# Optimization experiments

Measured on AMD Instinct MI355X. Metric: run time of the kernel, lower is better.

The kernel has to match this reference:

```python
import jax, jax.numpy as jnp
import numpy as np

EPS = 1e-5
HEAD_DIM = 2048 // 32  # embed_dim // num_heads -> scale factor only


def _layernorm(x, w):
    # torch: (x - mean) / sqrt(var_biased + eps) * w  (no bias)
    mean = jnp.mean(x, axis=-1, keepdims=True)
    var = jnp.var(x, axis=-1, keepdims=True)  # unbiased=False
    return w * ((x - mean) / jnp.sqrt(var + EPS))


def setup_inputs() -> dict:
    key = jax.random.key(0)
    ks = jax.random.split(key, 9)
    E, F, B, S = 2048, 8192, 2, 4096
    sE = 1.0 / np.sqrt(E)
    sF = 1.0 / np.sqrt(F)
    return {
        "x": jax.random.normal(ks[0], (B, S, E), jnp.float32),
        "ln_w": jnp.ones((E,), jnp.float32),
        "w_q": jax.random.normal(ks[1], (E, E), jnp.float32) * sE,
        "w_k": jax.random.normal(ks[2], (E, E), jnp.float32) * sE,
        "w_v": jax.random.normal(ks[3], (E, E), jnp.float32) * sE,
        "w_o": jax.random.normal(ks[4], (E, E), jnp.float32) * sE,
        "w_gate": jax.random.normal(ks[5], (E, F), jnp.float32) * sE,
        "w_up": jax.random.normal(ks[6], (E, F), jnp.float32) * sE,
        "w_down": jax.random.normal(ks[7], (F, E), jnp.float32) * sF,
    }


def reference(x, ln_w, w_q, w_k, w_v, w_o, w_gate, w_up, w_down):
    # --- pre-attention LN (uses input_layernorm weight) ---
    residual = x
    h = _layernorm(x, ln_w)  # [b, s, e]

    # --- attention exactly as written: transpose(1,2) WITHOUT head split ---
    q = jnp.einsum("bse,ef->bsf", h, w_q).swapaxes(1, 2)  # [b, e, s]
    k = jnp.einsum("bse,ef->bsf", h, w_k).swapaxes(1, 2)  # [b, e, s]
    v = jnp.einsum("bse,ef->bsf", h, w_v).swapaxes(1, 2)  # [b, e, s]
    # scores over the FEATURE axis: [b, e, e]
    scores = jnp.einsum("bes,bfs->bef", q, k) / np.sqrt(HEAD_DIM)
    weights = jax.nn.softmax(scores, axis=-1)
    attn = jnp.einsum("bef,bfs->bes", weights, v)  # [b, e, s]
    attn = attn.swapaxes(1, 2)  # [b, s, e]
    x = jnp.einsum("bse,ef->bsf", attn, w_o) + residual

    # --- pre-MLP LN: the module reuses input_layernorm here (faithful) ---
    residual = x
    h = _layernorm(x, ln_w)

    # --- GELU-gated FFN (exact erf gelu, torch default) ---
    gate = jax.nn.gelu(jnp.einsum("bse,ef->bsf", h, w_gate), approximate=False)
    up = jnp.einsum("bse,ef->bsf", h, w_up)
    out = jnp.einsum("bsf,fe->bse", gate * up, w_down) + residual
    return out
```

## Files before the change

### kernel.cpp

```cpp
#include <hip/hip_runtime.h>
#include <hip/hip_bf16.h>

typedef __hip_bfloat16 bf16;
typedef __attribute__((ext_vector_type(8))) short bf16x8;
typedef __attribute__((ext_vector_type(4))) float f32x4;

#define EPI_F32 0
#define EPI_BF16 1
#define EPI_BF16_T 2
#define EPI_F32_RES 3
#define EPI_BF16_GELU 4
#define EPI_BF16_MUL 5

__device__ __forceinline__ void gload_lds16(const void* g, void* l) {
  __builtin_amdgcn_global_load_lds(
      (const __attribute__((address_space(1))) unsigned int*)g,
      (__attribute__((address_space(3))) unsigned int*)l, 16, 0, 0);
}

template<int EPI>
__global__ __launch_bounds__(256, 3) void gemm_k(
    const bf16* __restrict__ A, const bf16* __restrict__ B,
    void* __restrict__ Cv, const void* __restrict__ auxv,
    int M, int N, int K, int lda, int ldb,
    long sAz, long sBz, long sCz, int batchM)
{
  __shared__ bf16 As[128 * 64];
  __shared__ bf16 Bs[128 * 64];

  const int z = blockIdx.z;
  A += (size_t)z * (size_t)sAz;
  B += (size_t)z * (size_t)sBz;

  const int brow = blockIdx.y * 128;
  const int bcol = blockIdx.x * 128;
  const int t = threadIdx.x;
  const int w = t >> 6;
  const int lane = t & 63;
  const int wr = (w >> 1) * 64;
  const int wc = (w & 1) * 64;
  const int l15 = lane & 15;
  const int lg = lane >> 4;

  f32x4 acc[4][4];
#pragma unroll
  for (int i = 0; i < 4; ++i)
#pragma unroll
    for (int j = 0; j < 4; ++j) {
      f32x4 zz = {0.f, 0.f, 0.f, 0.f};
      acc[i][j] = zz;
    }

  for (int kt = 0; kt < K; kt += 64) {
#pragma unroll
    for (int i = 0; i < 4; ++i) {
      const int bslot = (i * 4 + w) * 64;
      const int slot = bslot + lane;
      const int r = slot >> 3;
      const int cs = (slot & 7) ^ (r & 7);
      gload_lds16(A + (size_t)(brow + r) * lda + kt + cs * 8, (char*)As + bslot * 16);
      gload_lds16(B + (size_t)(bcol + r) * ldb + kt + cs * 8, (char*)Bs + bslot * 16);
    }
    __syncthreads();
#pragma unroll
    for (int ks = 0; ks < 2; ++ks) {
      bf16x8 av[4], bv[4];
#pragma unroll
      for (int mi = 0; mi < 4; ++mi) {
        const int r = wr + mi * 16 + l15;
        const int ch = (ks * 4 + lg) ^ (r & 7);
        av[mi] = *(const bf16x8*)((const char*)As + r * 128 + ch * 16);
      }
#pragma unroll
      for (int ni = 0; ni < 4; ++ni) {
        const int r = wc + ni * 16 + l15;
        const int ch = (ks * 4 + lg) ^ (r & 7);
        bv[ni] = *(const bf16x8*)((const char*)Bs + r * 128 + ch * 16);
      }
#pragma unroll
      for (int mi = 0; mi < 4; ++mi)
#pragma unroll
        for (int ni = 0; ni < 4; ++ni)
          acc[mi][ni] = __builtin_amdgcn_mfma_f32_16x16x32_bf16(av[mi], bv[ni], acc[mi][ni], 0, 0, 0);
    }
    __syncthreads();
  }

  if constexpr (EPI == EPI_BF16_T) {
    bf16* C = (bf16*)Cv + (size_t)z * (size_t)sCz;
#pragma unroll
    for (int mi = 0; mi < 4; ++mi) {
      const int mbase = brow + wr + mi * 16 + lg * 4;
      const int bi = mbase / batchM;
      const int ms = mbase - bi * batchM;
      const size_t base = (size_t)bi * (size_t)N * (size_t)batchM + (size_t)ms;
#pragma unroll
      for (int ni = 0; ni < 4; ++ni) {
        const int n = bcol + wc + ni * 16 + l15;
        bf16* p = C + base + (size_t)n * (size_t)batchM;
#pragma unroll
        for (int r = 0; r < 4; ++r) p[r] = __float2bfloat16(acc[mi][ni][r]);
      }
    }
  } else {
#pragma unroll
    for (int mi = 0; mi < 4; ++mi) {
#pragma unroll
      for (int r = 0; r < 4; ++r) {
        const int m = brow + wr + mi * 16 + lg * 4 + r;
#pragma unroll
        for (int ni = 0; ni < 4; ++ni) {
          const int n = bcol + wc + ni * 16 + l15;
          const size_t idx = (size_t)m * (size_t)N + (size_t)n;
          float v = acc[mi][ni][r];
          if constexpr (EPI == EPI_F32) {
            ((float*)Cv + (size_t)z * (size_t)sCz)[idx] = v;
          } else if constexpr (EPI == EPI_F32_RES) {
            ((float*)Cv)[idx] = v + ((const float*)auxv)[idx];
          } else if constexpr (EPI == EPI_BF16) {
            ((bf16*)Cv)[idx] = __float2bfloat16(v);
          } else if constexpr (EPI == EPI_BF16_GELU) {
            v = 0.5f * v * (1.0f + erff(v * 0.70710678118654752f));
            ((bf16*)Cv)[idx] = __float2bfloat16(v);
          } else if constexpr (EPI == EPI_BF16_MUL) {
            v = v * __bfloat162float(((const bf16*)auxv)[idx]);
            ((bf16*)Cv)[idx] = __float2bfloat16(v);
          }
        }
      }
    }
  }
}

__global__ __launch_bounds__(256) void ln_k(const float* __restrict__ x,
                                            const float* __restrict__ w,
                                            bf16* __restrict__ out) {
  const int row = blockIdx.x;
  const int t = threadIdx.x;
  const float* xr = x + (size_t)row * 2048;
  float4 a = ((const float4*)xr)[2 * t];
  float4 b = ((const float4*)xr)[2 * t + 1];
  float s = a.x + a.y + a.z + a.w + b.x + b.y + b.z + b.w;
  float ss = a.x * a.x + a.y * a.y + a.z * a.z + a.w * a.w +
             b.x * b.x + b.y * b.y + b.z * b.z + b.w * b.w;
#pragma unroll
  for (int o = 1; o < 64; o <<= 1) { s += __shfl_xor(s, o); ss += __shfl_xor(ss, o); }
  __shared__ float ps[4], pss[4];
  if ((t & 63) == 0) { ps[t >> 6] = s; pss[t >> 6] = ss; }
  __syncthreads();
  s = ps[0] + ps[1] + ps[2] + ps[3];
  ss = pss[0] + pss[1] + pss[2] + pss[3];
  const float mean = s * (1.0f / 2048.0f);
  const float var = ss * (1.0f / 2048.0f) - mean * mean;
  const float rstd = rsqrtf(var + 1e-5f);
  float4 wa = ((const float4*)w)[2 * t];
  float4 wb = ((const float4*)w)[2 * t + 1];
  bf16* o8 = out + (size_t)row * 2048 + (size_t)t * 8;
  o8[0] = __float2bfloat16((a.x - mean) * rstd * wa.x);
  o8[1] = __float2bfloat16((a.y - mean) * rstd * wa.y);
  o8[2] = __float2bfloat16((a.z - mean) * rstd * wa.z);
  o8[3] = __float2bfloat16((a.w - mean) * rstd * wa.w);
  o8[4] = __float2bfloat16((b.x - mean) * rstd * wb.x);
  o8[5] = __float2bfloat16((b.y - mean) * rstd * wb.y);
  o8[6] = __float2bfloat16((b.z - mean) * rstd * wb.z);
  o8[7] = __float2bfloat16((b.w - mean) * rstd * wb.w);
}

__global__ __launch_bounds__(256) void softmax_k(const float* __restrict__ sc,
                                                 bf16* __restrict__ o) {
  const int row = blockIdx.x;
  const int t = threadIdx.x;
  const float* sr = sc + (size_t)row * 2048;
  float4 a = ((const float4*)sr)[2 * t];
  float4 b = ((const float4*)sr)[2 * t + 1];
  float v[8] = {a.x, a.y, a.z, a.w, b.x, b.y, b.z, b.w};
  float m = -1e30f;
#pragma unroll
  for (int i = 0; i < 8; ++i) { v[i] *= 0.125f; m = fmaxf(m, v[i]); }
#pragma unroll
  for (int o2 = 1; o2 < 64; o2 <<= 1) m = fmaxf(m, __shfl_xor(m, o2));
  __shared__ float red[4];
  if ((t & 63) == 0) red[t >> 6] = m;
  __syncthreads();
  m = fmaxf(fmaxf(red[0], red[1]), fmaxf(red[2], red[3]));
  float sum = 0.f;
#pragma unroll
  for (int i = 0; i < 8; ++i) { v[i] = __expf(v[i] - m); sum += v[i]; }
#pragma unroll
  for (int o2 = 1; o2 < 64; o2 <<= 1) sum += __shfl_xor(sum, o2);
  __syncthreads();
  if ((t & 63) == 0) red[t >> 6] = sum;
  __syncthreads();
  sum = red[0] + red[1] + red[2] + red[3];
  const float inv = 1.0f / sum;
  bf16* po = o + (size_t)row * 2048 + (size_t)t * 8;
#pragma unroll
  for (int i = 0; i < 8; ++i) po[i] = __float2bfloat16(v[i] * inv);
}

__global__ __launch_bounds__(256) void transp_k(const float* __restrict__ in,
                                                bf16* __restrict__ out,
                                                int K, int N) {
  __shared__ float tile[32][33];
  const int bn = blockIdx.x * 32;
  const int bk = blockIdx.y * 32;
  const int tx = threadIdx.x;
  const int ty = threadIdx.y;
#pragma unroll
  for (int i = 0; i < 32; i += 8)
    tile[ty + i][tx] = in[(size_t)(bk + ty + i) * N + bn + tx];
  __syncthreads();
#pragma unroll
  for (int i = 0; i < 32; i += 8)
    out[(size_t)(bn + ty + i) * K + bk + tx] = __float2bfloat16(tile[tx][ty + i]);
}

extern "C" void kernel_launch(void* const* d_in, const int* in_sizes, int n_in,
                              void* d_out, int out_size, void* d_ws, size_t ws_size,
                              hipStream_t stream) {
  (void)in_sizes; (void)n_in; (void)out_size; (void)ws_size;
  const float* x   = (const float*)d_in[0];
  const float* lnw = (const float*)d_in[1];
  const float* w_q = (const float*)d_in[2];
  const float* w_k = (const float*)d_in[3];
  const float* w_v = (const float*)d_in[4];
  const float* w_o = (const float*)d_in[5];
  const float* w_g = (const float*)d_in[6];
  const float* w_u = (const float*)d_in[7];
  const float* w_d = (const float*)d_in[8];
  float* out = (float*)d_out;

  const int E = 2048, F = 8192;
  const size_t MB = 1024ull * 1024ull;
  char* ws = (char*)d_ws;

  bf16* wq_t = (bf16*)(ws + 0 * MB);
  bf16* wk_t = (bf16*)(ws + 8 * MB);
  bf16* wv_t = (bf16*)(ws + 16 * MB);
  bf16* wo_t = (bf16*)(ws + 24 * MB);
  bf16* wg_t = (bf16*)(ws + 32 * MB);
  bf16* wu_t = (bf16*)(ws + 64 * MB);
  bf16* wd_t = (bf16*)(ws + 96 * MB);
  bf16*  h      = (bf16*)(ws + 128 * MB);
  float* scores = (float*)(ws + 128 * MB);
  bf16*  h2     = (bf16*)(ws + 128 * MB);
  bf16*  qt    = (bf16*)(ws + 160 * MB);
  bf16*  attnT = (bf16*)(ws + 160 * MB);
  bf16*  kt  = (bf16*)(ws + 192 * MB);
  bf16*  wts = (bf16*)(ws + 192 * MB);
  bf16*  gc  = (bf16*)(ws + 192 * MB);
  bf16*  vm = (bf16*)(ws + 224 * MB);
  float* x2 = (float*)(ws + 224 * MB);

  dim3 blk(256), tb(32, 8);

  transp_k<<<dim3(E / 32, E / 32), tb, 0, stream>>>(w_q, wq_t, E, E);
  transp_k<<<dim3(E / 32, E / 32), tb, 0, stream>>>(w_k, wk_t, E, E);
  transp_k<<<dim3(E / 32, E / 32), tb, 0, stream>>>(w_v, wv_t, E, E);
  transp_k<<<dim3(E / 32, E / 32), tb, 0, stream>>>(w_o, wo_t, E, E);
  transp_k<<<dim3(F / 32, E / 32), tb, 0, stream>>>(w_g, wg_t, E, F);
  transp_k<<<dim3(F / 32, E / 32), tb, 0, stream>>>(w_u, wu_t, E, F);
  transp_k<<<dim3(E / 32, F / 32), tb, 0, stream>>>(w_d, wd_t, F, E);

  ln_k<<<8192, blk, 0, stream>>>(x, lnw, h);

  gemm_k<EPI_BF16_T><<<dim3(16, 64, 1), blk, 0, stream>>>(h, wq_t, qt, nullptr,
      8192, 2048, 2048, 2048, 2048, 0, 0, 0, 4096);
  gemm_k<EPI_BF16_T><<<dim3(16, 64, 1), blk, 0, stream>>>(h, wk_t, kt, nullptr,
      8192, 2048, 2048, 2048, 2048, 0, 0, 0, 4096);
  gemm_k<EPI_BF16><<<dim3(16, 64, 1), blk, 0, stream>>>(h, wv_t, vm, nullptr,
      8192, 2048, 2048, 2048, 2048, 0, 0, 0, 1);

  gemm_k<EPI_F32><<<dim3(16, 16, 2), blk, 0, stream>>>(qt, kt, scores, nullptr,
      2048, 2048, 4096, 4096, 4096, (long)2048 * 4096, (long)2048 * 4096,
      (long)2048 * 2048, 1);

  softmax_k<<<4096, blk, 0, stream>>>(scores, wts);

  gemm_k<EPI_BF16_T><<<dim3(32, 16, 2), blk, 0, stream>>>(wts, vm, attnT, nullptr,
      2048, 4096, 2048, 2048, 2048, (long)2048 * 2048, (long)4096 * 2048,
      (long)4096 * 2048, 2048);

  gemm_k<EPI_F32_RES><<<dim3(16, 64, 1), blk, 0, stream>>>(attnT, wo_t, x2, x,
      8192, 2048, 2048, 2048, 2048, 0, 0, 0, 1);

  ln_k<<<8192, blk, 0, stream>>>(x2, lnw, h2);

  for (int c = 0; c < 4; ++c) {
    gemm_k<EPI_BF16_GELU><<<dim3(16, 64, 1), blk, 0, stream>>>(
        h2, wg_t + (size_t)c * 2048 * 2048, gc, nullptr,
        8192, 2048, 2048, 2048, 2048, 0, 0, 0, 1);
    gemm_k<EPI_BF16_MUL><<<dim3(16, 64, 1), blk, 0, stream>>>(
        h2, wu_t + (size_t)c * 2048 * 2048, gc, gc,
        8192, 2048, 2048, 2048, 2048, 0, 0, 0, 1);
    gemm_k<EPI_F32_RES><<<dim3(16, 64, 1), blk, 0, stream>>>(
        gc, wd_t + (size_t)c * 2048, out,
        (c == 0 ? (const void*)x2 : (const void*)out),
        8192, 2048, 2048, 2048, 8192, 0, 0, 0, 1);
  }
}
```

Baseline: 1.540 ms.

## Replace 128x128 GEMM with pipelined 256x256 tile kernel and split-K scores

Replaces the 128x128 single-buffered GEMM with a 512-thread 256x256 tile kernel. The new kernel double-buffers LDS, prefetches two K-tiles ahead, interleaves LDS reads with MFMA at raised wave priority, and remaps block IDs into groups of eight. The scores GEMM is split along K into two partial buffers that the softmax adds together, which doubles parallelism for that small-output GEMM. FFN chunks double in width (two chunks instead of four) and the transposed epilogue writes 4-wide vectors. The larger tiles and 128 KB of LDS lower occupancy and leave fewer blocks for load balancing.

```diff
diff --git a/kernel.cpp b/kernel.cpp
--- a/kernel.cpp
+++ b/kernel.cpp
@@ -5,116 +5,170 @@
 typedef __attribute__((ext_vector_type(8))) short bf16x8;
 typedef __attribute__((ext_vector_type(4))) float f32x4;
 
-#define EPI_F32 0
 #define EPI_BF16 1
 #define EPI_BF16_T 2
 #define EPI_F32_RES 3
 #define EPI_BF16_GELU 4
 #define EPI_BF16_MUL 5
-
-__device__ __forceinline__ void gload_lds16(const void* g, void* l) {
+#define EPI_F32_KSPLIT 6
+
+__device__ __forceinline__ void gload_lds16(const bf16* g, char* l) {
   __builtin_amdgcn_global_load_lds(
       (const __attribute__((address_space(1))) unsigned int*)g,
       (__attribute__((address_space(3))) unsigned int*)l, 16, 0, 0);
 }
 
+#define SCHED0() __builtin_amdgcn_sched_barrier(0)
+
+#define MFQ(Q, AR)                                                                 \
+  do {                                                                             \
+    __builtin_amdgcn_s_setprio(1);                                                 \
+    _Pragma("unroll") for (int j_ = 0; j_ < 2; ++j_)                               \
+        _Pragma("unroll") for (int ni_ = 0; ni_ < 4; ++ni_)                        \
+            _Pragma("unroll") for (int ks_ = 0; ks_ < 2; ++ks_)                    \
+                acc[(Q) * 2 + j_][ni_] = __builtin_amdgcn_mfma_f32_16x16x32_bf16(  \
+                    AR[j_][ks_], bfr[ni_][ks_], acc[(Q) * 2 + j_][ni_], 0, 0, 0);  \
+    __builtin_amdgcn_s_setprio(0);                                                 \
+  } while (0)
+
 template<int EPI>
-__global__ __launch_bounds__(256, 3) void gemm_k(
+__global__ __launch_bounds__(512, 2) void gemm256_k(
     const bf16* __restrict__ A, const bf16* __restrict__ B,
     void* __restrict__ Cv, const void* __restrict__ auxv,
-    int M, int N, int K, int lda, int ldb,
+    int N, int K, int lda, int ldb,
     long sAz, long sBz, long sCz, int batchM)
 {
-  __shared__ bf16 As[128 * 64];
-  __shared__ bf16 Bs[128 * 64];
-
-  const int z = blockIdx.z;
-  A += (size_t)z * (size_t)sAz;
-  B += (size_t)z * (size_t)sBz;
-
-  const int brow = blockIdx.y * 128;
-  const int bcol = blockIdx.x * 128;
+  __shared__ bf16 lds[4 * 256 * 64];
+  char* const As0 = (char*)lds;
+  char* const Bs0 = As0 + 32768;
+  char* const As1 = Bs0 + 32768;
+  char* const Bs1 = As1 + 32768;
+
+  const int gx = gridDim.x, gy = gridDim.y;
+  int lid = (blockIdx.z * gy + blockIdx.y) * gx + blockIdx.x;
+  const int cpx = (gx * gy * gridDim.z) >> 3;
+  lid = (lid & 7) * cpx + (lid >> 3);
+  const int bx = lid % gx;
+  const int rem = lid / gx;
+  const int by = rem % gy;
+  const int z = rem / gy;
+
+  int zb = z, part = 0;
+  if constexpr (EPI == EPI_F32_KSPLIT) { zb = z & 1; part = z >> 1; }
+  A += (size_t)zb * (size_t)sAz + (size_t)part * (size_t)batchM;
+  B += (size_t)zb * (size_t)sBz + (size_t)part * (size_t)batchM;
+
+  const int brow = by * 256, bcol = bx * 256;
   const int t = threadIdx.x;
-  const int w = t >> 6;
-  const int lane = t & 63;
-  const int wr = (w >> 1) * 64;
-  const int wc = (w & 1) * 64;
-  const int l15 = lane & 15;
-  const int lg = lane >> 4;
-
-  f32x4 acc[4][4];
-#pragma unroll
-  for (int i = 0; i < 4; ++i)
+  const int w = t >> 6, lane = t & 63;
+  const int wrow = (w >> 2) * 128;
+  const int wcol = (w & 3) * 64;
+  const int l15 = lane & 15, lg = lane >> 4;
+
+  f32x4 acc[8][4];
+#pragma unroll
+  for (int i = 0; i < 8; ++i)
 #pragma unroll
     for (int j = 0; j < 4; ++j) {
       f32x4 zz = {0.f, 0.f, 0.f, 0.f};
       acc[i][j] = zz;
     }
 
-  for (int kt = 0; kt < K; kt += 64) {
+  auto STAGE = [&](int kk, char* Ad, char* Bd) {
 #pragma unroll
     for (int i = 0; i < 4; ++i) {
-      const int bslot = (i * 4 + w) * 64;
+      const int bslot = (i * 8 + w) * 64;
       const int slot = bslot + lane;
       const int r = slot >> 3;
       const int cs = (slot & 7) ^ (r & 7);
-      gload_lds16(A + (size_t)(brow + r) * lda + kt + cs * 8, (char*)As + bslot * 16);
-      gload_lds16(B + (size_t)(bcol + r) * ldb + kt + cs * 8, (char*)Bs + bslot * 16);
+      gload_lds16(A + (size_t)(brow + r) * lda + kk + cs * 8, Ad + bslot * 16);
+      gload_lds16(B + (size_t)(bcol + r) * ldb + kk + cs * 8, Bd + bslot * 16);
     }
-    __syncthreads();
-#pragma unroll
-    for (int ks = 0; ks < 2; ++ks) {
-      bf16x8 av[4], bv[4];
-#pragma unroll
-      for (int mi = 0; mi < 4; ++mi) {
-        const int r = wr + mi * 16 + l15;
-        const int ch = (ks * 4 + lg) ^ (r & 7);
-        av[mi] = *(const bf16x8*)((const char*)As + r * 128 + ch * 16);
-      }
-#pragma unroll
-      for (int ni = 0; ni < 4; ++ni) {
-        const int r = wc + ni * 16 + l15;
-        const int ch = (ks * 4 + lg) ^ (r & 7);
-        bv[ni] = *(const bf16x8*)((const char*)Bs + r * 128 + ch * 16);
-      }
-#pragma unroll
-      for (int mi = 0; mi < 4; ++mi)
-#pragma unroll
-        for (int ni = 0; ni < 4; ++ni)
-          acc[mi][ni] = __builtin_amdgcn_mfma_f32_16x16x32_bf16(av[mi], bv[ni], acc[mi][ni], 0, 0, 0);
-    }
-    __syncthreads();
+  };
+  auto rdA = [&](const char* Ab, int mi, int ks) {
+    const int r = wrow + mi * 16 + l15;
+    return *(const bf16x8*)(Ab + ((r * 8 + ((ks * 4 + lg) ^ (r & 7))) << 4));
+  };
+  auto rdB = [&](const char* Bb, int ni, int ks) {
+    const int r = wcol + ni * 16 + l15;
+    return *(const bf16x8*)(Bb + ((r * 8 + ((ks * 4 + lg) ^ (r & 7))) << 4));
+  };
+
+  STAGE(0, As0, Bs0);
+  STAGE(64, As1, Bs1);
+
+  const int NT = K >> 6;
+  bf16x8 bfr[4][2], aA[2][2], aB[2][2];
+
+  for (int tt = 0; tt < NT; ++tt) {
+    const char* Ar = (tt & 1) ? As1 : As0;
+    const char* Br = (tt & 1) ? Bs1 : Bs0;
+    char* Aw = (tt & 1) ? As1 : As0;
+    char* Bw = (tt & 1) ? Bs1 : Bs0;
+
+    if (tt + 1 < NT) { asm volatile("s_waitcnt vmcnt(8)" ::: "memory"); }
+    else             { asm volatile("s_waitcnt vmcnt(0)" ::: "memory"); }
+    SCHED0();
+    __builtin_amdgcn_s_barrier();
+    SCHED0();
+
+    bfr[0][0] = rdB(Br, 0, 0); bfr[0][1] = rdB(Br, 0, 1);
+    bfr[1][0] = rdB(Br, 1, 0); bfr[1][1] = rdB(Br, 1, 1);
+    bfr[2][0] = rdB(Br, 2, 0); bfr[2][1] = rdB(Br, 2, 1);
+    bfr[3][0] = rdB(Br, 3, 0); bfr[3][1] = rdB(Br, 3, 1);
+    aA[0][0] = rdA(Ar, 0, 0); aA[0][1] = rdA(Ar, 0, 1);
+    aA[1][0] = rdA(Ar, 1, 0); aA[1][1] = rdA(Ar, 1, 1);
+    aB[0][0] = rdA(Ar, 2, 0); aB[0][1] = rdA(Ar, 2, 1);
+    aB[1][0] = rdA(Ar, 3, 0); aB[1][1] = rdA(Ar, 3, 1);
+    MFQ(0, aA);
+    aA[0][0] = rdA(Ar, 4, 0); aA[0][1] = rdA(Ar, 4, 1);
+    aA[1][0] = rdA(Ar, 5, 0); aA[1][1] = rdA(Ar, 5, 1);
+    MFQ(1, aB);
+    aB[0][0] = rdA(Ar, 6, 0); aB[0][1] = rdA(Ar, 6, 1);
+    aB[1][0] = rdA(Ar, 7, 0); aB[1][1] = rdA(Ar, 7, 1);
+    MFQ(2, aA);
+    asm volatile("s_waitcnt lgkmcnt(0)" ::: "memory");
+    SCHED0();
+    __builtin_amdgcn_s_barrier();
+    SCHED0();
+    if (tt + 2 < NT) STAGE((tt + 2) * 64, Aw, Bw);
+    MFQ(3, aB);
   }
 
   if constexpr (EPI == EPI_BF16_T) {
-    bf16* C = (bf16*)Cv + (size_t)z * (size_t)sCz;
-#pragma unroll
-    for (int mi = 0; mi < 4; ++mi) {
-      const int mbase = brow + wr + mi * 16 + lg * 4;
+    bf16* C = (bf16*)Cv + (size_t)zb * (size_t)sCz;
+#pragma unroll
+    for (int mi = 0; mi < 8; ++mi) {
+      const int mbase = brow + wrow + mi * 16 + lg * 4;
       const int bi = mbase / batchM;
       const int ms = mbase - bi * batchM;
       const size_t base = (size_t)bi * (size_t)N * (size_t)batchM + (size_t)ms;
 #pragma unroll
       for (int ni = 0; ni < 4; ++ni) {
-        const int n = bcol + wc + ni * 16 + l15;
-        bf16* p = C + base + (size_t)n * (size_t)batchM;
-#pragma unroll
-        for (int r = 0; r < 4; ++r) p[r] = __float2bfloat16(acc[mi][ni][r]);
+        const int n = bcol + wcol + ni * 16 + l15;
+        union { short4 s; short h[4]; } u;
+#pragma unroll
+        for (int r = 0; r < 4; ++r) {
+          bf16 bv = __float2bfloat16(acc[mi][ni][r]);
+          u.h[r] = *(short*)&bv;
+        }
+        *(short4*)(C + base + (size_t)n * (size_t)batchM) = u.s;
       }
     }
   } else {
 #pragma unroll
-    for (int mi = 0; mi < 4; ++mi) {
+    for (int mi = 0; mi < 8; ++mi) {
 #pragma unroll
       for (int r = 0; r < 4; ++r) {
-        const int m = brow + wr + mi * 16 + lg * 4 + r;
+        const int m = brow + wrow + mi * 16 + lg * 4 + r;
 #pragma unroll
         for (int ni = 0; ni < 4; ++ni) {
-          const int n = bcol + wc + ni * 16 + l15;
+          const int n = bcol + wcol + ni * 16 + l15;
           const size_t idx = (size_t)m * (size_t)N + (size_t)n;
           float v = acc[mi][ni][r];
-          if constexpr (EPI == EPI_F32) {
-            ((float*)Cv + (size_t)z * (size_t)sCz)[idx] = v;
+          if constexpr (EPI == EPI_F32_KSPLIT) {
+            float* C = (part ? (float*)auxv : (float*)Cv) + (size_t)zb * (size_t)sCz;
+            C[idx] = v;
           } else if constexpr (EPI == EPI_F32_RES) {
             ((float*)Cv)[idx] = v + ((const float*)auxv)[idx];
           } else if constexpr (EPI == EPI_BF16) {
@@ -166,14 +220,19 @@
   o8[7] = __float2bfloat16((b.w - mean) * rstd * wb.w);
 }
 
-__global__ __launch_bounds__(256) void softmax_k(const float* __restrict__ sc,
-                                                 bf16* __restrict__ o) {
+__global__ __launch_bounds__(256) void softmax2_k(const float* __restrict__ s0,
+                                                  const float* __restrict__ s1,
+                                                  bf16* __restrict__ o) {
   const int row = blockIdx.x;
   const int t = threadIdx.x;
-  const float* sr = sc + (size_t)row * 2048;
-  float4 a = ((const float4*)sr)[2 * t];
-  float4 b = ((const float4*)sr)[2 * t + 1];
-  float v[8] = {a.x, a.y, a.z, a.w, b.x, b.y, b.z, b.w};
+  const float* r0 = s0 + (size_t)row * 2048;
+  const float* r1 = s1 + (size_t)row * 2048;
+  float4 a = ((const float4*)r0)[2 * t];
+  float4 b = ((const float4*)r0)[2 * t + 1];
+  float4 c = ((const float4*)r1)[2 * t];
+  float4 d = ((const float4*)r1)[2 * t + 1];
+  float v[8] = {a.x + c.x, a.y + c.y, a.z + c.z, a.w + c.w,
+                b.x + d.x, b.y + d.y, b.z + d.z, b.w + d.w};
   float m = -1e30f;
 #pragma unroll
   for (int i = 0; i < 8; ++i) { v[i] *= 0.125f; m = fmaxf(m, v[i]); }
@@ -241,18 +300,19 @@
   bf16* wg_t = (bf16*)(ws + 32 * MB);
   bf16* wu_t = (bf16*)(ws + 64 * MB);
   bf16* wd_t = (bf16*)(ws + 96 * MB);
-  bf16*  h      = (bf16*)(ws + 128 * MB);
-  float* scores = (float*)(ws + 128 * MB);
-  bf16*  h2     = (bf16*)(ws + 128 * MB);
+  bf16*  h   = (bf16*)(ws + 128 * MB);
+  float* sp0 = (float*)(ws + 128 * MB);
+  bf16*  h2  = (bf16*)(ws + 128 * MB);
   bf16*  qt    = (bf16*)(ws + 160 * MB);
   bf16*  attnT = (bf16*)(ws + 160 * MB);
+  bf16*  gc    = (bf16*)(ws + 160 * MB);
   bf16*  kt  = (bf16*)(ws + 192 * MB);
   bf16*  wts = (bf16*)(ws + 192 * MB);
-  bf16*  gc  = (bf16*)(ws + 192 * MB);
-  bf16*  vm = (bf16*)(ws + 224 * MB);
-  float* x2 = (float*)(ws + 224 * MB);
-
-  dim3 blk(256), tb(32, 8);
+  bf16*  vm  = (bf16*)(ws + 224 * MB);
+  float* x2  = (float*)(ws + 224 * MB);
+  float* sp1 = (float*)(ws + 256 * MB);
+
+  dim3 blk(256), tb(32, 8), g512(512);
 
   transp_k<<<dim3(E / 32, E / 32), tb, 0, stream>>>(w_q, wq_t, E, E);
   transp_k<<<dim3(E / 32, E / 32), tb, 0, stream>>>(w_k, wk_t, E, E);
@@ -264,38 +324,38 @@
 
   ln_k<<<8192, blk, 0, stream>>>(x, lnw, h);
 
-  gemm_k<EPI_BF16_T><<<dim3(16, 64, 1), blk, 0, stream>>>(h, wq_t, qt, nullptr,
-      8192, 2048, 2048, 2048, 2048, 0, 0, 0, 4096);
-  gemm_k<EPI_BF16_T><<<dim3(16, 64, 1), blk, 0, stream>>>(h, wk_t, kt, nullptr,
-      8192, 2048, 2048, 2048, 2048, 0, 0, 0, 4096);
-  gemm_k<EPI_BF16><<<dim3(16, 64, 1), blk, 0, stream>>>(h, wv_t, vm, nullptr,
-      8192, 2048, 2048, 2048, 2048, 0, 0, 0, 1);
-
-  gemm_k<EPI_F32><<<dim3(16, 16, 2), blk, 0, stream>>>(qt, kt, scores, nullptr,
-      2048, 2048, 4096, 4096, 4096, (long)2048 * 4096, (long)2048 * 4096,
-      (long)2048 * 2048, 1);
-
-  softmax_k<<<4096, blk, 0, stream>>>(scores, wts);
-
-  gemm_k<EPI_BF16_T><<<dim3(32, 16, 2), blk, 0, stream>>>(wts, vm, attnT, nullptr,
-      2048, 4096, 2048, 2048, 2048, (long)2048 * 2048, (long)4096 * 2048,
+  gemm256_k<EPI_BF16_T><<<dim3(8, 32, 1), g512, 0, stream>>>(h, wq_t, qt, nullptr,
+      2048, 2048, 2048, 2048, 0, 0, 0, 4096);
+  gemm256_k<EPI_BF16_T><<<dim3(8, 32, 1), g512, 0, stream>>>(h, wk_t, kt, nullptr,
+      2048, 2048, 2048, 2048, 0, 0, 0, 4096);
+  gemm256_k<EPI_BF16><<<dim3(8, 32, 1), g512, 0, stream>>>(h, wv_t, vm, nullptr,
+      2048, 2048, 2048, 2048, 0, 0, 0, 1);
+
+  gemm256_k<EPI_F32_KSPLIT><<<dim3(8, 8, 4), g512, 0, stream>>>(qt, kt, sp0, sp1,
+      2048, 2048, 4096, 4096, (long)2048 * 4096, (long)2048 * 4096,
+      (long)2048 * 2048, 2048);
+
+  softmax2_k<<<4096, blk, 0, stream>>>(sp0, sp1, wts);
+
+  gemm256_k<EPI_BF16_T><<<dim3(16, 8, 2), g512, 0, stream>>>(wts, vm, attnT, nullptr,
+      4096, 2048, 2048, 2048, (long)2048 * 2048, (long)4096 * 2048,
       (long)4096 * 2048, 2048);
 
-  gemm_k<EPI_F32_RES><<<dim3(16, 64, 1), blk, 0, stream>>>(attnT, wo_t, x2, x,
-      8192, 2048, 2048, 2048, 2048, 0, 0, 0, 1);
+  gemm256_k<EPI_F32_RES><<<dim3(8, 32, 1), g512, 0, stream>>>(attnT, wo_t, x2, x,
+      2048, 2048, 2048, 2048, 0, 0, 0, 1);
 
   ln_k<<<8192, blk, 0, stream>>>(x2, lnw, h2);
 
-  for (int c = 0; c < 4; ++c) {
-    gemm_k<EPI_BF16_GELU><<<dim3(16, 64, 1), blk, 0, stream>>>(
-        h2, wg_t + (size_t)c * 2048 * 2048, gc, nullptr,
-        8192, 2048, 2048, 2048, 2048, 0, 0, 0, 1);
-    gemm_k<EPI_BF16_MUL><<<dim3(16, 64, 1), blk, 0, stream>>>(
-        h2, wu_t + (size_t)c * 2048 * 2048, gc, gc,
-        8192, 2048, 2048, 2048, 2048, 0, 0, 0, 1);
-    gemm_k<EPI_F32_RES><<<dim3(16, 64, 1), blk, 0, stream>>>(
-        gc, wd_t + (size_t)c * 2048, out,
+  for (int c = 0; c < 2; ++c) {
+    gemm256_k<EPI_BF16_GELU><<<dim3(16, 32, 1), g512, 0, stream>>>(
+        h2, wg_t + (size_t)c * 4096 * 2048, gc, nullptr,
+        4096, 2048, 2048, 2048, 0, 0, 0, 1);
+    gemm256_k<EPI_BF16_MUL><<<dim3(16, 32, 1), g512, 0, stream>>>(
+        h2, wu_t + (size_t)c * 4096 * 2048, gc, gc,
+        4096, 2048, 2048, 2048, 0, 0, 0, 1);
+    gemm256_k<EPI_F32_RES><<<dim3(8, 32, 1), g512, 0, stream>>>(
+        gc, wd_t + (size_t)c * 4096, out,
         (c == 0 ? (const void*)x2 : (const void*)out),
-        8192, 2048, 2048, 2048, 8192, 0, 0, 0, 1);
+        2048, 4096, 4096, 8192, 0, 0, 0, 1);
   }
 }
```

Result: faster. 1.426 ms (-7.4%).
